# Kernel optimization log

Measured on AMD Instinct MI355X. Metric: run time of the kernel, lower is better.

Reference implementation:

```python
import jax, jax.numpy as jnp
import numpy as np

N, S, Q, P = 100000, 64, 50, 3  # pauli words, heads, qubits, pauli basis
EPS = 1e-12  # F.normalize clamp


def setup_inputs() -> dict:
    key = jax.random.key(0)
    k1, k2, k3, k4 = jax.random.split(key, 4)
    return {
        "batch_pauli_tensor": jax.random.uniform(k1, (N, Q, P), dtype=jnp.float32),
        "batch_coeff": jax.random.normal(k2, (N,), dtype=jnp.float32),
        "heads_param": jax.random.normal(k3, (S, Q, P), dtype=jnp.float32),
        "head_ratios_param": jax.random.normal(k4, (S,), dtype=jnp.float32),
    }


def reference(batch_pauli_tensor, batch_coeff, heads_param, head_ratios_param):
    s = heads_param.shape[0]
    heads = jax.nn.softplus(heads_param * 20.0)
    heads = heads / jnp.maximum(jnp.sum(heads, axis=-1, keepdims=True), EPS)
    hr = jax.nn.softplus(head_ratios_param * 20.0)
    hr = hr / jnp.maximum(jnp.sum(hr), EPS)
    hr = (hr + 0.001 / s) / 1.001
    # coverage: per-(word, head, qubit) match prob -> product over qubits -> ratio-weighted sum
    cov = jnp.einsum('nqp,sqp->nsq', batch_pauli_tensor, heads)  # [n, s, q]
    cov = jnp.prod(cov, axis=-1)                                 # [n, s]
    cov = jnp.einsum('s,ns->n', hr, cov)                         # [n]
    # variance loss
    return jnp.sum(batch_coeff ** 2 / cov)
```

## Files before the change

### kernel.cpp

```cpp
#include <hip/hip_runtime.h>
#include <math.h>

#define N_Q 50
#define N_P 3
#define N_S 64
#define ROW 150
#define BLK_ROWS 64
#define THREADS 256
#define WAVES 4
#define SCHUNK 16

#define WS_CNT_OFF 12544
#define WS_HP_OFF 12608
#define WS_HRV_OFF 51008

__device__ __forceinline__ float softplus20(float x) {
    float z = x * 20.0f;
    return fmaxf(z, 0.0f) + log1pf(expf(-fabsf(z)));
}

__global__ void precompute_kernel(const float* __restrict__ heads_param,
                                  const float* __restrict__ hr_param,
                                  float* __restrict__ HP,
                                  float* __restrict__ hrv,
                                  int* __restrict__ cnt) {
    const int tid = threadIdx.x;
    if (blockIdx.x == 0) {
        if (tid == 0) *cnt = 0;
        if (tid < N_S) {
            float sp = softplus20(hr_param[tid]);
            float tot = sp;
            #pragma unroll
            for (int off = 32; off; off >>= 1) tot += __shfl_xor(tot, off);
            float hr = sp / fmaxf(tot, 1e-12f);
            hrv[tid] = (hr + 0.001f / (float)N_S) / 1.001f;
        }
    }
    int idx = blockIdx.x * blockDim.x + tid;
    if (idx < N_S * N_Q) {
        int q = idx / N_S;
        int s = idx - q * N_S;
        const float* hp = heads_param + ((size_t)s * N_Q + q) * N_P;
        float sp0 = softplus20(hp[0]);
        float sp1 = softplus20(hp[1]);
        float sp2 = softplus20(hp[2]);
        float denom = fmaxf(sp0 + sp1 + sp2, 1e-12f);
        float* o = HP + ((size_t)q * N_S + s) * 3;
        o[0] = sp0 / denom;
        o[1] = sp1 / denom;
        o[2] = sp2 / denom;
    }
}

__device__ __forceinline__ void computeQ1(const float4* __restrict__ Hq,
                                          float a0, float a1, float a2,
                                          float (&p)[SCHUNK]) {
    #pragma unroll
    for (int g = 0; g < 4; ++g) {
        float4 b0 = Hq[3 * g], b1 = Hq[3 * g + 1], b2 = Hq[3 * g + 2];
        p[4*g+0] *= fmaf(b0.x, a0, fmaf(b0.y, a1, b0.z * a2));
        p[4*g+1] *= fmaf(b0.w, a0, fmaf(b1.x, a1, b1.y * a2));
        p[4*g+2] *= fmaf(b1.z, a0, fmaf(b1.w, a1, b2.x * a2));
        p[4*g+3] *= fmaf(b2.y, a0, fmaf(b2.z, a1, b2.w * a2));
    }
}

__global__ __launch_bounds__(THREADS) void main_kernel(
    const float* __restrict__ A, const float* __restrict__ coeff,
    const float* __restrict__ HP, const float* __restrict__ hrv,
    double* __restrict__ partials, int* __restrict__ cnt,
    float* __restrict__ out, int N) {
    __shared__ float covs[WAVES][BLK_ROWS];
    __shared__ double redf[WAVES];
    __shared__ int isLast;

    const int tid = threadIdx.x;
    const int lane = tid & 63;
    const int wave = tid >> 6;
    const int wq = __builtin_amdgcn_readfirstlane(wave);
    const int nbase = blockIdx.x * BLK_ROWS;

    int n0 = nbase + lane;  if (n0 >= N) n0 = N - 1;
    const float2* __restrict__ pA0 = (const float2*)A + (size_t)n0 * (ROW / 2);

    float prod[SCHUNK];
    #pragma unroll
    for (int i = 0; i < SCHUNK; ++i) prod[i] = 1.0f;

    const float4* __restrict__ Hw = (const float4*)HP + 12 * wq;

    float2 x0 = pA0[0], x1 = pA0[1], x2 = pA0[2];

    #pragma unroll 5
    for (int w = 0; w < N_Q / 2; ++w) {
        const int nb = (w < N_Q / 2 - 1) ? 3 * w + 3 : 0;
        float2 nx0 = pA0[nb], nx1 = pA0[nb + 1], nx2 = pA0[nb + 2];
        const float4* Hq = Hw + 96 * w;
        computeQ1(Hq,      x0.x, x0.y, x1.x, prod);
        computeQ1(Hq + 48, x1.y, x2.x, x2.y, prod);
        x0 = nx0; x1 = nx1; x2 = nx2;
    }

    float acc = 0.0f;
    const float* __restrict__ hw = hrv + SCHUNK * wq;
    #pragma unroll
    for (int i = 0; i < SCHUNK; ++i) acc = fmaf(hw[i], prod[i], acc);
    covs[wave][lane] = acc;
    __syncthreads();

    double td = 0.0;
    if (wave == 0) {
        float cov = covs[0][lane] + covs[1][lane] + covs[2][lane] + covs[3][lane];
        float term = 0.0f;
        int n = nbase + lane;
        if (n < N) { float c = coeff[n]; term = (c * c) / cov; }
        td = (double)term;
        #pragma unroll
        for (int off = 32; off; off >>= 1) td += __shfl_down(td, off);
    }

    if (tid == 0) {
        partials[blockIdx.x] = td;
        __threadfence();
        int v = atomicAdd(cnt, 1);
        isLast = (v == (int)gridDim.x - 1);
    }
    __syncthreads();

    if (isLast) {
        __threadfence();
        double s = 0.0;
        for (int i = tid; i < (int)gridDim.x; i += THREADS) s += partials[i];
        #pragma unroll
        for (int off = 32; off; off >>= 1) s += __shfl_down(s, off);
        if (lane == 0) redf[wave] = s;
        __syncthreads();
        if (tid == 0) {
            double t = 0.0;
            #pragma unroll
            for (int wv = 0; wv < WAVES; ++wv) t += redf[wv];
            out[0] = (float)t;
        }
    }
}

extern "C" void kernel_launch(void* const* d_in, const int* in_sizes, int n_in,
                              void* d_out, int out_size, void* d_ws, size_t ws_size,
                              hipStream_t stream) {
    const float* A           = (const float*)d_in[0];
    const float* coeff       = (const float*)d_in[1];
    const float* heads_param = (const float*)d_in[2];
    const float* hr_param    = (const float*)d_in[3];
    const int N = in_sizes[1];
    const int nblocks = (N + BLK_ROWS - 1) / BLK_ROWS;

    char* ws = (char*)d_ws;
    double* partials = (double*)ws;
    int*   cnt = (int*)(ws + WS_CNT_OFF);
    float* HP  = (float*)(ws + WS_HP_OFF);
    float* hrv = (float*)(ws + WS_HRV_OFF);
    float* out = (float*)d_out;

    const int pre_blocks = (N_S * N_Q + THREADS - 1) / THREADS;
    precompute_kernel<<<pre_blocks, THREADS, 0, stream>>>(heads_param, hr_param,
                                                          HP, hrv, cnt);
    main_kernel<<<nblocks, THREADS, 0, stream>>>(A, coeff, HP, hrv, partials,
                                                 cnt, out, N);
}
```

Before: 155.8 us.

## Map lanes to heads with head params in registers, stream rows wave-uniformly

Swaps the work mapping. Each lane now owns one head and keeps all 150 of its normalized head parameters in registers. Each wave walks 16 rows, loading row data at wave-uniform addresses, double-buffered in 15-float chunks, and processes two rows at a time. Per-head products go to LDS, where 16 lanes apply the head-ratio weighted sum and the coefficient term, followed by a per-block reduction. This removes the 4x redundant per-lane row reads and the repeated head-parameter loads. The costs are heavy register pressure (launch bounds set to 2 blocks) and only two dependent product chains per lane, which lowers instruction-level parallelism.

```diff
diff --git a/kernel.cpp b/kernel.cpp
--- a/kernel.cpp
+++ b/kernel.cpp
@@ -8,7 +8,7 @@
 #define BLK_ROWS 64
 #define THREADS 256
 #define WAVES 4
-#define SCHUNK 16
+#define RPW 16
 
 #define WS_CNT_OFF 12544
 #define WS_HP_OFF 12608
@@ -52,75 +52,114 @@
     }
 }
 
-__device__ __forceinline__ void computeQ1(const float4* __restrict__ Hq,
-                                          float a0, float a1, float a2,
-                                          float (&p)[SCHUNK]) {
+template<int CH>
+__device__ __forceinline__ void loadc(const float* __restrict__ p, float (&b)[15]) {
     #pragma unroll
-    for (int g = 0; g < 4; ++g) {
-        float4 b0 = Hq[3 * g], b1 = Hq[3 * g + 1], b2 = Hq[3 * g + 2];
-        p[4*g+0] *= fmaf(b0.x, a0, fmaf(b0.y, a1, b0.z * a2));
-        p[4*g+1] *= fmaf(b0.w, a0, fmaf(b1.x, a1, b1.y * a2));
-        p[4*g+2] *= fmaf(b1.z, a0, fmaf(b1.w, a1, b2.x * a2));
-        p[4*g+3] *= fmaf(b2.y, a0, fmaf(b2.z, a1, b2.w * a2));
-    }
-}
-
-__global__ __launch_bounds__(THREADS) void main_kernel(
+    for (int k = 0; k < 15; ++k) b[k] = p[CH * 15 + k];
+}
+
+template<int C>
+__device__ __forceinline__ void chunk5(const float (&h)[N_Q][N_P],
+                                       const float (&b)[15], float& prod) {
+    #pragma unroll
+    for (int j = 0; j < 5; ++j) {
+        float t = h[5 * C + j][2] * b[3 * j + 2];
+        t = fmaf(h[5 * C + j][1], b[3 * j + 1], t);
+        t = fmaf(h[5 * C + j][0], b[3 * j + 0], t);
+        prod *= t;
+    }
+}
+
+__global__ __launch_bounds__(THREADS, 2) void main_kernel(
     const float* __restrict__ A, const float* __restrict__ coeff,
     const float* __restrict__ HP, const float* __restrict__ hrv,
     double* __restrict__ partials, int* __restrict__ cnt,
     float* __restrict__ out, int N) {
-    __shared__ float covs[WAVES][BLK_ROWS];
+    __shared__ float plds[WAVES][RPW][N_S + 1];
     __shared__ double redf[WAVES];
     __shared__ int isLast;
 
     const int tid = threadIdx.x;
     const int lane = tid & 63;
-    const int wave = tid >> 6;
-    const int wq = __builtin_amdgcn_readfirstlane(wave);
-    const int nbase = blockIdx.x * BLK_ROWS;
-
-    int n0 = nbase + lane;  if (n0 >= N) n0 = N - 1;
-    const float2* __restrict__ pA0 = (const float2*)A + (size_t)n0 * (ROW / 2);
-
-    float prod[SCHUNK];
+    const int wq = __builtin_amdgcn_readfirstlane(tid >> 6);
+    const int wbase = blockIdx.x * BLK_ROWS + RPW * wq;
+
+    float h[N_Q][N_P];
+    {
+        const float* __restrict__ HPl = HP + 3 * lane;
+        #pragma unroll
+        for (int q = 0; q < N_Q; ++q) {
+            h[q][0] = HPl[q * (N_S * 3) + 0];
+            h[q][1] = HPl[q * (N_S * 3) + 1];
+            h[q][2] = HPl[q * (N_S * 3) + 2];
+        }
+    }
+
+    float a0[15], a1[15], b0[15], b1[15];
+    {
+        const int nA = min(wbase + 0, N - 1);
+        const int nB = min(wbase + 8, N - 1);
+        const float* pa = A + (size_t)nA * ROW;
+        const float* pb = A + (size_t)nB * ROW;
+        loadc<0>(pa, a0); loadc<0>(pb, b0);
+        loadc<1>(pa, a1); loadc<1>(pb, b1);
+    }
+
+    for (int rp = 0; rp < 8; ++rp) {
+        const int nA = min(wbase + rp, N - 1);
+        const int nB = min(wbase + 8 + rp, N - 1);
+        const float* pa = A + (size_t)nA * ROW;
+        const float* pb = A + (size_t)nB * ROW;
+        const float* panA = A + (size_t)min(nA + 1, N - 1) * ROW;
+        const float* panB = A + (size_t)min(nB + 1, N - 1) * ROW;
+
+        float prodA = 1.0f, prodB = 1.0f;
+        chunk5<0>(h, a0, prodA); loadc<2>(pa, a0);
+        chunk5<0>(h, b0, prodB); loadc<2>(pb, b0);
+        chunk5<1>(h, a1, prodA); loadc<3>(pa, a1);
+        chunk5<1>(h, b1, prodB); loadc<3>(pb, b1);
+        chunk5<2>(h, a0, prodA); loadc<4>(pa, a0);
+        chunk5<2>(h, b0, prodB); loadc<4>(pb, b0);
+        chunk5<3>(h, a1, prodA); loadc<5>(pa, a1);
+        chunk5<3>(h, b1, prodB); loadc<5>(pb, b1);
+        chunk5<4>(h, a0, prodA); loadc<6>(pa, a0);
+        chunk5<4>(h, b0, prodB); loadc<6>(pb, b0);
+        chunk5<5>(h, a1, prodA); loadc<7>(pa, a1);
+        chunk5<5>(h, b1, prodB); loadc<7>(pb, b1);
+        chunk5<6>(h, a0, prodA); loadc<8>(pa, a0);
+        chunk5<6>(h, b0, prodB); loadc<8>(pb, b0);
+        chunk5<7>(h, a1, prodA); loadc<9>(pa, a1);
+        chunk5<7>(h, b1, prodB); loadc<9>(pb, b1);
+        chunk5<8>(h, a0, prodA); loadc<0>(panA, a0);
+        chunk5<8>(h, b0, prodB); loadc<0>(panB, b0);
+        chunk5<9>(h, a1, prodA); loadc<1>(panA, a1);
+        chunk5<9>(h, b1, prodB); loadc<1>(panB, b1);
+
+        plds[wq][rp][lane] = prodA;
+        plds[wq][8 + rp][lane] = prodB;
+    }
+
+    double td = 0.0;
+    if (lane < RPW) {
+        float acc0 = 0.0f, acc1 = 0.0f, acc2 = 0.0f, acc3 = 0.0f;
+        #pragma unroll
+        for (int i = 0; i < 16; ++i) {
+            acc0 = fmaf(hrv[i],      plds[wq][lane][i],      acc0);
+            acc1 = fmaf(hrv[i + 16], plds[wq][lane][i + 16], acc1);
+            acc2 = fmaf(hrv[i + 32], plds[wq][lane][i + 32], acc2);
+            acc3 = fmaf(hrv[i + 48], plds[wq][lane][i + 48], acc3);
+        }
+        float cov = ((acc0 + acc1) + acc2) + acc3;
+        int n = wbase + lane;
+        if (n < N) { float c = coeff[n]; td = (double)((c * c) / cov); }
+    }
     #pragma unroll
-    for (int i = 0; i < SCHUNK; ++i) prod[i] = 1.0f;
-
-    const float4* __restrict__ Hw = (const float4*)HP + 12 * wq;
-
-    float2 x0 = pA0[0], x1 = pA0[1], x2 = pA0[2];
-
-    #pragma unroll 5
-    for (int w = 0; w < N_Q / 2; ++w) {
-        const int nb = (w < N_Q / 2 - 1) ? 3 * w + 3 : 0;
-        float2 nx0 = pA0[nb], nx1 = pA0[nb + 1], nx2 = pA0[nb + 2];
-        const float4* Hq = Hw + 96 * w;
-        computeQ1(Hq,      x0.x, x0.y, x1.x, prod);
-        computeQ1(Hq + 48, x1.y, x2.x, x2.y, prod);
-        x0 = nx0; x1 = nx1; x2 = nx2;
-    }
-
-    float acc = 0.0f;
-    const float* __restrict__ hw = hrv + SCHUNK * wq;
-    #pragma unroll
-    for (int i = 0; i < SCHUNK; ++i) acc = fmaf(hw[i], prod[i], acc);
-    covs[wave][lane] = acc;
+    for (int off = 32; off; off >>= 1) td += __shfl_down(td, off);
+    if (lane == 0) redf[wq] = td;
     __syncthreads();
 
-    double td = 0.0;
-    if (wave == 0) {
-        float cov = covs[0][lane] + covs[1][lane] + covs[2][lane] + covs[3][lane];
-        float term = 0.0f;
-        int n = nbase + lane;
-        if (n < N) { float c = coeff[n]; term = (c * c) / cov; }
-        td = (double)term;
-        #pragma unroll
-        for (int off = 32; off; off >>= 1) td += __shfl_down(td, off);
-    }
-
     if (tid == 0) {
-        partials[blockIdx.x] = td;
+        partials[blockIdx.x] = ((redf[0] + redf[1]) + redf[2]) + redf[3];
         __threadfence();
         int v = atomicAdd(cnt, 1);
         isLast = (v == (int)gridDim.x - 1);
@@ -133,14 +172,10 @@
         for (int i = tid; i < (int)gridDim.x; i += THREADS) s += partials[i];
         #pragma unroll
         for (int off = 32; off; off >>= 1) s += __shfl_down(s, off);
-        if (lane == 0) redf[wave] = s;
+        __shared__ double redg[WAVES];
+        if (lane == 0) redg[tid >> 6] = s;
         __syncthreads();
-        if (tid == 0) {
-            double t = 0.0;
-            #pragma unroll
-            for (int wv = 0; wv < WAVES; ++wv) t += redf[wv];
-            out[0] = (float)t;
-        }
+        if (tid == 0) out[0] = (float)(((redg[0] + redg[1]) + redg[2]) + redg[3]);
     }
 }
 
```

New measurement: 249.5 us. 1.6x slower.
